# Kernel optimization log

Measured on AMD Instinct MI355X. Metric: run time of the kernel, lower is better.

## Reference

```python
import jax, jax.numpy as jnp
import numpy as np

B, S_IN, T_OUT, H, L, V = 64, 512, 64, 1024, 2, 1024


def setup_inputs() -> dict:
    key = jax.random.key(0)
    ks = iter(jax.random.split(key, 64))
    def p(shape, scale=0.02):
        return (jax.random.normal(next(ks), shape, jnp.float32) * scale)
    d = {"x": jax.random.normal(next(ks), (B, 2, S_IN), jnp.float32)}
    d["emb"] = p((V, H))
    for l in range(L):
        i = 2 if l == 0 else H
        d[f"enc_Wih{l}"] = p((3 * H, i)); d[f"enc_Whh{l}"] = p((3 * H, H))
        d[f"enc_bih{l}"] = p((3 * H,));   d[f"enc_bhh{l}"] = p((3 * H,))
        d[f"dec_Wih{l}"] = p((H, H));     d[f"dec_Whh{l}"] = p((H, H))
        d[f"dec_bih{l}"] = p((H,));       d[f"dec_bhh{l}"] = p((H,))
    d["hq_W"] = p((H, H)); d["hq_b"] = p((H,))
    d["comb_W"] = p((H, 2 * H)); d["comb_b"] = p((H,))
    d["fc_W"] = p((V, H)); d["fc_b"] = p((V,))
    return d


def _gru_layer(x_seq, Wih, Whh, bih, bhh):
    # x_seq: [B,T,I] -> (outputs [B,T,H], h_T [B,H]). PyTorch GRU gate order r,z,n.
    xp = jnp.einsum('bti,gi->btg', x_seq, Wih) + bih  # [B,T,3H]
    h0 = jnp.zeros((x_seq.shape[0], Whh.shape[1]), x_seq.dtype)
    def step(h, xpt):
        hp = h @ Whh.T + bhh
        xr, xz, xn = jnp.split(xpt, 3, axis=-1)
        hr, hz, hn = jnp.split(hp, 3, axis=-1)
        r = jax.nn.sigmoid(xr + hr)
        z = jax.nn.sigmoid(xz + hz)
        n = jnp.tanh(xn + r * hn)
        h = (1.0 - z) * n + z * h
        return h, h
    hT, ys = jax.lax.scan(step, h0, jnp.swapaxes(xp, 0, 1))
    return jnp.swapaxes(ys, 0, 1), hT


def _forward(x, emb,
             enc_Wih0, enc_Whh0, enc_bih0, enc_bhh0,
             enc_Wih1, enc_Whh1, enc_bih1, enc_bhh1,
             dec_Wih0, dec_Whh0, dec_bih0, dec_bhh0,
             dec_Wih1, dec_Whh1, dec_bih1, dec_bhh1,
             hq_W, hq_b, comb_W, comb_b, fc_W, fc_b):
    enc_params = [(enc_Wih0, enc_Whh0, enc_bih0, enc_bhh0),
                  (enc_Wih1, enc_Whh1, enc_bih1, enc_bhh1)]
    dec_params = [(dec_Wih0, dec_Whh0, dec_bih0, dec_bhh0),
                  (dec_Wih1, dec_Whh1, dec_bih1, dec_bhh1)]
    # ---- encoder: GRU over x permuted to [B, S_in, 2] ----
    seq = jnp.transpose(x, (0, 2, 1)).astype(jnp.float32)
    h_enc = []
    for (Wih, Whh, bih, bhh) in enc_params:
        seq, hT = _gru_layer(seq, Wih, Whh, bih, bhh)
        h_enc.append(hT)
    enc_outs = seq                      # [B, S_in, H]
    hidden0 = jnp.stack(h_enc, axis=0)  # [L, B, H]

    tok0 = jnp.zeros((B,), jnp.int32)
    def dec_step(carry, _):
        tok, hid = carry
        inp = emb[tok]                  # [B, H]
        new_h = []
        for l, (Wih, Whh, bih, bhh) in enumerate(dec_params):
            h = jnp.tanh(inp @ Wih.T + bih + hid[l] @ Whh.T + bhh)
            new_h.append(h)
            inp = h
        hid = jnp.stack(new_h, axis=0)
        q = inp @ hq_W.T + hq_b                          # [B, H]
        scores = jnp.einsum('bsh,bh->bs', enc_outs, q)   # [B, S_in]
        aw = jax.nn.softmax(scores, axis=1)
        att = jnp.einsum('bs,bsh->bh', aw, enc_outs)     # [B, H]
        logits = jnp.concatenate([inp, att], axis=-1) @ comb_W.T + comb_b
        logits = logits @ fc_W.T + fc_b                  # [B, V]
        tok = jnp.argmax(logits, axis=-1).astype(jnp.int32)
        return (tok, hid), (logits, aw)
    (_, hidden), (logits_t, aw_t) = jax.lax.scan(dec_step, (tok0, hidden0), None, length=T_OUT)
    vec_out = jnp.swapaxes(logits_t, 0, 1)   # [B, T_out, V]
    attn = aw_t[-1][:, None, :]              # [B, 1, S_in] (last step, as in source)
    return vec_out, hidden, attn


def reference(x, emb,
              enc_Wih0, enc_Whh0, enc_bih0, enc_bhh0,
              enc_Wih1, enc_Whh1, enc_bih1, enc_bhh1,
              dec_Wih0, dec_Whh0, dec_bih0, dec_bhh0,
              dec_Wih1, dec_Whh1, dec_bih1, dec_bhh1,
              hq_W, hq_b, comb_W, comb_b, fc_W, fc_b):
    return _forward(x, emb,
                    enc_Wih0, enc_Whh0, enc_bih0, enc_bhh0,
                    enc_Wih1, enc_Whh1, enc_bih1, enc_bhh1,
                    dec_Wih0, dec_Whh0, dec_bih0, dec_bhh0,
                    dec_Wih1, dec_Whh1, dec_bih1, dec_bhh1,
                    hq_W, hq_b, comb_W, comb_b, fc_W, fc_b)
```

## Files before the change

### kernel.cpp

```cpp
#include <hip/hip_runtime.h>
#include <stdint.h>


#define BB 64
#define SS 512
#define TT 64
#define HH 1024
#define VV 1024
#define BH 65536
#define SH 524288
#define OFF_HID  4194304
#define OFF_ATTN 4325376

typedef _Float16 half8  __attribute__((ext_vector_type(8)));
typedef float    floatx4 __attribute__((ext_vector_type(4)));

struct P {
  const float *x, *emb;
  const float *eWih0, *eWhh0, *ebih0, *ebhh0;
  const float *dWih0, *dWhh0, *dbih0, *dbhh0;
  const float *eWih1, *eWhh1, *ebih1, *ebhh1;
  const float *dWih1, *dWhh1, *dbih1, *dbhh1;
  const float *hqW, *hqb, *combW, *combb, *fcW, *fcb;
  uint32_t* enc_i;
  _Float16 *W0h,*W0l;
  _Float16 *W1h,*W1l;
  _Float16 *embh,*embl,*T0h,*T0l;
  _Float16 *wih0dh,*wih0dl,*wih1dh,*wih1dl,*whh0dh,*whh0dl,*whh1dh,*whh1dl;
  _Float16 *hqh,*hql,*combh,*combl,*fch,*fcl;
  _Float16 *h0h,*h0l,*h1h,*h1l;
  _Float16 *dh0h,*dh0l,*dh1h,*dh1l;
  _Float16 *cath,*catl;
  _Float16 *ch,*cl;
  float *u0,*u1,*w1x,*q;
  float *attp_o;
  float *attp_ml;
  float *sc63;
  unsigned long long* amax;
  float* dout;
};

struct GSet { const _Float16 *Wh, *Wl, *Ah, *Al; const float *bias; float *out; };

__device__ __forceinline__ void splitf(float x, _Float16& hi, _Float16& lo){
  _Float16 h = (_Float16)x; hi = h;
  lo = (_Float16)((x - (float)h) * 2048.0f);
}
__device__ __forceinline__ float reconf(_Float16 hi, _Float16 lo){
  return fmaf((float)lo, 1.0f/2048.0f, (float)hi);
}
__device__ __forceinline__ float recon_u32(uint32_t w){
  float hi = (float)__builtin_bit_cast(_Float16, (unsigned short)(w & 0xffffu));
  float lo = (float)__builtin_bit_cast(_Float16, (unsigned short)(w >> 16));
  return fmaf(lo, 1.0f/2048.0f, hi);
}
__device__ __forceinline__ uint32_t pack_pair(float x){
  _Float16 hi, lo; splitf(x, hi, lo);
  return (uint32_t)__builtin_bit_cast(unsigned short, hi)
       | ((uint32_t)__builtin_bit_cast(unsigned short, lo) << 16);
}
__device__ __forceinline__ unsigned ordf(float f){
  unsigned u = __float_as_uint(f);
  return (u & 0x80000000u) ? ~u : (u | 0x80000000u);
}

template<int NT, int KH, bool SPLIT>
__device__ __forceinline__ void gemm_core(
    const _Float16* __restrict__ Ah0, const _Float16* __restrict__ Al0,
    const _Float16* __restrict__ Ah1, const _Float16* __restrict__ Al1,
    int sA,
    const _Float16* __restrict__ Wh, const _Float16* __restrict__ Wl,
    int nrows, _Float16* ldsW, float* accOut)
{
  const int tid = threadIdx.x, lane = tid & 63, wave = tid >> 6;
  const int mA = (wave<<4) + (lane & 15);
  const int kb = ((lane>>4) << 3);
  const int wstride = KH << 10;
  floatx4 aH[NT], aM1[NT], aM2[NT];
  int ne[NT];
  const _Float16* bh_base[NT];
  const _Float16* bl_base[NT];
  #pragma unroll
  for (int nt=0; nt<NT; ++nt){
    int nn = (lane & 15) + (nt<<4);
    ne[nt] = nn < nrows ? nn : nrows - 1;
    bh_base[nt] = ldsW + ne[nt]*1032 + kb;
    aH[nt]  = floatx4{0.f,0.f,0.f,0.f};
    aM1[nt] = floatx4{0.f,0.f,0.f,0.f};
    aM2[nt] = floatx4{0.f,0.f,0.f,0.f};
  }
  #pragma unroll
  for (int kh=0; kh<KH; ++kh){
    __syncthreads();
    const int iters = (nrows*128 + 255) >> 8;
    for (int it=0; it<iters; ++it){
      int idx = tid + (it<<8);
      int row = idx >> 7, col = (idx & 127) << 3;
      if (row < nrows)
        *(half8*)(ldsW + row*1032 + col) =
            *(const half8*)(Wh + row*wstride + (kh<<10) + col);
    }
    __syncthreads();
    const _Float16* ah_p = ((KH==2 && kh==1) ? Ah1 : Ah0) + mA*sA + kb;
    const _Float16* al_p = ((KH==2 && kh==1) ? Al1 : Al0) + mA*sA + kb;
    #pragma unroll
    for (int nt=0; nt<NT; ++nt) bl_base[nt] = Wl + ne[nt]*wstride + (kh<<10) + kb;
    #pragma unroll 4
    for (int ks=0; ks<32; ++ks){
      half8 ah = *(const half8*)(ah_p + (ks<<5));
      half8 al = *(const half8*)(al_p + (ks<<5));
      #pragma unroll
      for (int nt=0; nt<NT; ++nt){
        half8 bh = *(const half8*)(bh_base[nt] + (ks<<5));
        half8 bl = *(const half8*)(bl_base[nt] + (ks<<5));
        aH[nt]  = __builtin_amdgcn_mfma_f32_16x16x32_f16(ah, bh, aH[nt],  0,0,0);
        aM1[nt] = __builtin_amdgcn_mfma_f32_16x16x32_f16(ah, bl, aM1[nt], 0,0,0);
        aM2[nt] = __builtin_amdgcn_mfma_f32_16x16x32_f16(al, bh, aM2[nt], 0,0,0);
      }
    }
    if (SPLIT){
      #pragma unroll
      for (int nt=0; nt<NT; ++nt){
        #pragma unroll
        for (int r=0;r<4;++r)
          accOut[(kh*NT + nt)*4 + r] = aH[nt][r] + (aM1[nt][r] + aM2[nt][r]) * (1.f/2048.f);
        aH[nt]  = floatx4{0.f,0.f,0.f,0.f};
        aM1[nt] = floatx4{0.f,0.f,0.f,0.f};
        aM2[nt] = floatx4{0.f,0.f,0.f,0.f};
      }
    }
  }
  if (!SPLIT){
    #pragma unroll
    for (int nt=0; nt<NT; ++nt)
      #pragma unroll
      for (int r=0;r<4;++r)
        accOut[nt*4 + r] = aH[nt][r] + (aM1[nt][r] + aM2[nt][r]) * (1.f/2048.f);
  }
}

__global__ __launch_bounds__(256) void k_split(const float* __restrict__ src,
                                               _Float16* dh, _Float16* dl, int n){
  for (int i = blockIdx.x*256 + threadIdx.x; i < n; i += gridDim.x*256){
    _Float16 hi,lo; splitf(src[i],hi,lo); dh[i]=hi; dl[i]=lo;
  }
}

__global__ __launch_bounds__(256) void k_rw0(P p){
  const int n = 128*24*1024;
  for (int i = blockIdx.x*256 + threadIdx.x; i < n; i += gridDim.x*256){
    int k = i & 1023; int rest = i >> 10; int rr = rest % 24; int blk = rest / 24;
    int grow = (rr>>3)*1024 + (blk<<3) + (rr&7);
    _Float16 hi,lo; splitf(p.eWhh0[grow*1024 + k],hi,lo);
    p.W0h[i]=hi; p.W0l[i]=lo;
  }
}
__global__ __launch_bounds__(256) void k_rw1(P p){
  const int n = 128*24*2048;
  for (int i = blockIdx.x*256 + threadIdx.x; i < n; i += gridDim.x*256){
    int k = i & 2047; int rest = i >> 11; int rr = rest % 24; int blk = rest / 24;
    int grow = (rr>>3)*1024 + (blk<<3) + (rr&7);
    float v = (k < 1024) ? p.eWhh1[grow*1024 + k] : p.eWih1[grow*1024 + (k-1024)];
    _Float16 hi,lo; splitf(v,hi,lo);
    p.W1h[i]=hi; p.W1l[i]=lo;
  }
}
__global__ __launch_bounds__(256) void k_zero(P p){
  int i = blockIdx.x*256 + threadIdx.x;
  p.h1h[i] = (_Float16)0.f; p.h1l[i] = (_Float16)0.f;
  p.h0h[BH + i] = (_Float16)0.f; p.h0l[BH + i] = (_Float16)0.f;
}
__global__ __launch_bounds__(256) void k_t0(P p){
  __shared__ _Float16 ldsW[16*1032];
  const int ns = blockIdx.x & 63, mc = blockIdx.x >> 6;
  float acc[4];
  gemm_core<1,1,false>(p.embh + mc*65536, p.embl + mc*65536, nullptr, nullptr, 1024,
                       p.wih0dh + ns*16*1024, p.wih0dl + ns*16*1024, 16, ldsW, acc);
  const int lane = threadIdx.x & 63, wave = threadIdx.x >> 6;
  const int n = lane & 15, col = (ns<<4) + n;
  const float bv = p.dbih0[col];
  #pragma unroll
  for (int r=0;r<4;++r){
    int v = mc*64 + (wave<<4) + ((lane>>4)<<2) + r;
    _Float16 hi,lo; splitf(acc[r] + bv, hi, lo);
    p.T0h[v*1024 + col] = hi; p.T0l[v*1024 + col] = lo;
  }
}

__global__ __launch_bounds__(256) void k_enc(P p, int e){
  const int tid = threadIdx.x, lane = tid & 63, wave = tid >> 6;
  const bool is0 = blockIdx.x < 128;
  if (is0 && e >= 512) return;
  if (!is0 && e < 1) return;
  const int blk = is0 ? blockIdx.x : blockIdx.x - 128;
  const int j0 = blk << 3;

  __shared__ _Float16 ldsW[24*1032];
  __shared__ float ldsG[2][24][68];
  __shared__ float ldsC[24][4];

  if (tid < 24){
    int grow = (tid>>3)*1024 + j0 + (tid & 7);
    if (is0){
      ldsC[tid][0] = p.eWih0[grow*2+0];
      ldsC[tid][1] = p.eWih0[grow*2+1];
      ldsC[tid][2] = p.ebih0[grow];
      ldsC[tid][3] = p.ebhh0[grow];
    } else {
      ldsC[tid][0] = p.ebih1[grow];
      ldsC[tid][1] = p.ebhh1[grow];
    }
  }

  const int cur = e & 1, prv = cur ^ 1;
  float acc[16];
  if (is0){
    gemm_core<2,1,true>(p.h0h + prv*BH, p.h0l + prv*BH, nullptr, nullptr, 1024,
                        p.W0h + blk*24*1024, p.W0l + blk*24*1024, 24, ldsW, acc);
    #pragma unroll
    for (int nt=0; nt<2; ++nt){
      int n = (lane & 15) + (nt<<4);
      if (n < 24){
        #pragma unroll
        for (int r=0;r<4;++r)
          ldsG[0][n][(wave<<4)+((lane>>4)<<2)+r] = acc[nt*4+r];
      }
    }
  } else {
    gemm_core<2,2,true>(p.h1h + prv*BH, p.h1l + prv*BH,
                        p.h0h + prv*BH, p.h0l + prv*BH, 1024,
                        p.W1h + blk*24*2048, p.W1l + blk*24*2048, 24, ldsW, acc);
    #pragma unroll
    for (int kh=0; kh<2; ++kh){
      #pragma unroll
      for (int nt=0; nt<2; ++nt){
        int n = (lane & 15) + (nt<<4);
        if (n < 24){
          #pragma unroll
          for (int r=0;r<4;++r)
            ldsG[kh][n][(wave<<4)+((lane>>4)<<2)+r] = acc[(kh*2+nt)*4+r];
        }
      }
    }
  }
  __syncthreads();

  #pragma unroll
  for (int it=0; it<2; ++it){
    int idx = tid + (it<<8);
    int b = idx & 63, j = idx >> 6;
    int col = j0 + j;
    if (is0){
      int t = e;
      float hr = ldsG[0][j][b]    + ldsC[j][3];
      float hz = ldsG[0][8+j][b]  + ldsC[8+j][3];
      float hn = ldsG[0][16+j][b] + ldsC[16+j][3];
      float x0 = p.x[b*1024 + t], x1 = p.x[b*1024 + 512 + t];
      float xr = fmaf(x0, ldsC[j][0],    fmaf(x1, ldsC[j][1],    ldsC[j][2]));
      float xz = fmaf(x0, ldsC[8+j][0],  fmaf(x1, ldsC[8+j][1],  ldsC[8+j][2]));
      float xn = fmaf(x0, ldsC[16+j][0], fmaf(x1, ldsC[16+j][1], ldsC[16+j][2]));
      float rg = 1.0f/(1.0f + expf(-(xr+hr)));
      float zg = 1.0f/(1.0f + expf(-(xz+hz)));
      float ng = tanhf(xn + rg*hn);
      float hold = reconf(p.h0h[prv*BH + b*1024 + col], p.h0l[prv*BH + b*1024 + col]);
      float hnew = (1.0f - zg)*ng + zg*hold;
      _Float16 hi,lo; splitf(hnew,hi,lo);
      p.h0h[cur*BH + b*1024 + col] = hi;
      p.h0l[cur*BH + b*1024 + col] = lo;
    } else {
      int t = e - 1;
      float hr = ldsG[0][j][b]    + ldsC[j][1];
      float hz = ldsG[0][8+j][b]  + ldsC[8+j][1];
      float hn = ldsG[0][16+j][b] + ldsC[16+j][1];
      float xr = ldsG[1][j][b]    + ldsC[j][0];
      float xz = ldsG[1][8+j][b]  + ldsC[8+j][0];
      float xn = ldsG[1][16+j][b] + ldsC[16+j][0];
      float rg = 1.0f/(1.0f + expf(-(xr+hr)));
      float zg = 1.0f/(1.0f + expf(-(xz+hz)));
      float ng = tanhf(xn + rg*hn);
      float hold = reconf(p.h1h[prv*BH + b*1024 + col], p.h1l[prv*BH + b*1024 + col]);
      float hnew = (1.0f - zg)*ng + zg*hold;
      _Float16 hi,lo; splitf(hnew,hi,lo);
      p.h1h[cur*BH + b*1024 + col] = hi;
      p.h1l[cur*BH + b*1024 + col] = lo;
      p.enc_i[b*SH + t*1024 + col] = pack_pair(hnew);
    }
  }
}

__global__ __launch_bounds__(256) void k_dgemm2(GSet a, GSet b){
  const int tid = threadIdx.x, lane = tid & 63, wave = tid >> 6;
  const GSet g = blockIdx.x < 128 ? a : b;
  const int blk = blockIdx.x & 127;
  __shared__ _Float16 ldsW[8*1032];
  float acc[4];
  gemm_core<1,1,false>(g.Ah, g.Al, nullptr, nullptr, 1024,
                       g.Wh + blk*8*1024, g.Wl + blk*8*1024, 8, ldsW, acc);
  int n = lane & 15;
  if (n < 8){
    int col = (blk<<3) + n;
    float bv = g.bias[col];
    #pragma unroll
    for (int r=0;r<4;++r){
      int m = (wave<<4)+((lane>>4)<<2)+r;
      g.out[m*1024 + col] = acc[r] + bv;
    }
  }
}

__global__ __launch_bounds__(256) void k_dec0(P p, int t){
  const int tid = threadIdx.x, b = blockIdx.x;
  __shared__ unsigned long long red[256];
  unsigned long long v = 0;
  if (t > 0 && tid < 128) v = p.amax[b*128 + tid];
  red[tid] = v; __syncthreads();
  for (int off=128; off>=1; off>>=1){
    if (tid < off){ unsigned long long o = red[tid+off]; if (o > red[tid]) red[tid] = o; }
    __syncthreads();
  }
  const int tokb = (t > 0) ? (1023 - (int)(red[0] & 0xffffffffULL)) : 0;
  #pragma unroll
  for (int i=0;i<4;++i){
    int h = tid + (i<<8);
    float val = tanhf(reconf(p.T0h[tokb*1024+h], p.T0l[tokb*1024+h]) + p.u0[b*1024+h]);
    _Float16 hi,lo; splitf(val,hi,lo);
    p.dh0h[b*1024+h]=hi; p.dh0l[b*1024+h]=lo;
  }
}
__global__ __launch_bounds__(256) void k_dec2(P p){
  const int tid = threadIdx.x, b = blockIdx.x;
  #pragma unroll
  for (int i=0;i<4;++i){
    int h = tid + (i<<8);
    float val = tanhf(p.w1x[b*1024+h] + p.u1[b*1024+h]);
    _Float16 hi,lo; splitf(val,hi,lo);
    p.dh1h[b*1024+h]=hi; p.dh1l[b*1024+h]=lo;
    p.cath[b*2048+h]=hi; p.catl[b*2048+h]=lo;
  }
}
__global__ __launch_bounds__(256) void k_flash(P p, int t){
  const int tid = threadIdx.x, lane = tid & 63, wave = tid >> 6;
  const int b = blockIdx.x >> 1, half = blockIdx.x & 1;
  const int s0 = half << 8;
  const bool last = (t == 63);
  float qv[16];
  #pragma unroll
  for (int i=0;i<16;++i) qv[i] = p.q[b*1024 + (i<<6) + lane];
  float ov[16];
  #pragma unroll
  for (int i=0;i<16;++i) ov[i] = 0.f;
  float mrun = -3.0e38f, lrun = 0.f;
  for (int si=0; si<64; ++si){
    int s = s0 + (wave<<6) + si;
    const uint32_t* ep = p.enc_i + b*SH + s*1024 + lane;
    float ef[16]; float partial = 0.f;
    #pragma unroll
    for (int i=0;i<16;++i){
      ef[i] = recon_u32(ep[i<<6]);
      partial = fmaf(ef[i], qv[i], partial);
    }
    #pragma unroll
    for (int off=32; off; off>>=1) partial += __shfl_xor(partial, off, 64);
    if (last && lane == 0) p.sc63[b*512 + s] = partial;
    float mnew = fmaxf(mrun, partial);
    float fac = __expf(mrun - mnew);
    float w   = __expf(partial - mnew);
    lrun = fmaf(lrun, fac, w);
    #pragma unroll
    for (int i=0;i<16;++i) ov[i] = fmaf(ov[i], fac, w*ef[i]);
    mrun = mnew;
  }
  __shared__ float ldsO[4][1024];
  __shared__ float ldsM[4], ldsL2[4];
  #pragma unroll
  for (int i=0;i<16;++i) ldsO[wave][(i<<6)+lane] = ov[i];
  if (lane == 0){ ldsM[wave] = mrun; ldsL2[wave] = lrun; }
  __syncthreads();
  float M = fmaxf(fmaxf(ldsM[0],ldsM[1]), fmaxf(ldsM[2],ldsM[3]));
  float f0 = __expf(ldsM[0]-M), f1 = __expf(ldsM[1]-M),
        f2 = __expf(ldsM[2]-M), f3 = __expf(ldsM[3]-M);
  if (tid == 0){
    p.attp_ml[b*4 + half*2 + 0] = M;
    p.attp_ml[b*4 + half*2 + 1] = f0*ldsL2[0] + f1*ldsL2[1] + f2*ldsL2[2] + f3*ldsL2[3];
  }
  #pragma unroll
  for (int i=0;i<4;++i){
    int h = tid + (i<<8);
    p.attp_o[(b*2+half)*1024 + h] =
        f0*ldsO[0][h] + f1*ldsO[1][h] + f2*ldsO[2][h] + f3*ldsO[3][h];
  }
}
__global__ __launch_bounds__(256) void k_dec5(P p, int t){
  const int tid = threadIdx.x, b = blockIdx.x;
  float m0 = p.attp_ml[b*4+0], l0 = p.attp_ml[b*4+1];
  float m1 = p.attp_ml[b*4+2], l1 = p.attp_ml[b*4+3];
  float M = fmaxf(m0,m1);
  float f0 = expf(m0-M), f1 = expf(m1-M);
  float invL = 1.0f/(f0*l0 + f1*l1);
  #pragma unroll
  for (int i=0;i<4;++i){
    int h = tid + (i<<8);
    float o = (f0*p.attp_o[(b*2+0)*1024+h] + f1*p.attp_o[(b*2+1)*1024+h]) * invL;
    _Float16 hi,lo; splitf(o,hi,lo);
    p.cath[b*2048 + 1024 + h] = hi; p.catl[b*2048 + 1024 + h] = lo;
  }
  if (t == 63){
    #pragma unroll
    for (int i=0;i<2;++i){
      int s = tid + (i<<8);
      p.dout[OFF_ATTN + b*512 + s] = expf(p.sc63[b*512+s] - M) * invL;
    }
  }
}
__global__ __launch_bounds__(256) void k_comb(P p){
  const int tid = threadIdx.x, lane = tid & 63, wave = tid >> 6;
  const int blk = blockIdx.x;
  __shared__ _Float16 ldsW[8*1032];
  float acc[4];
  gemm_core<1,2,false>(p.cath, p.catl, p.cath + 1024, p.catl + 1024, 2048,
                       p.combh + blk*8*2048, p.combl + blk*8*2048, 8, ldsW, acc);
  int n = lane & 15;
  if (n < 8){
    int col = (blk<<3) + n;
    float bv = p.combb[col];
    #pragma unroll
    for (int r=0;r<4;++r){
      int m = (wave<<4)+((lane>>4)<<2)+r;
      _Float16 hi,lo; splitf(acc[r] + bv, hi, lo);
      p.ch[m*1024 + col] = hi; p.cl[m*1024 + col] = lo;
    }
  }
}
__global__ __launch_bounds__(256) void k_fc(P p, int t){
  const int tid = threadIdx.x, lane = tid & 63, wave = tid >> 6;
  const int blk = blockIdx.x;
  __shared__ _Float16 ldsW[8*1032];
  __shared__ float ldsL[8][68];
  float acc[4];
  gemm_core<1,1,false>(p.ch, p.cl, nullptr, nullptr, 1024,
                       p.fch + blk*8*1024, p.fcl + blk*8*1024, 8, ldsW, acc);
  int n = lane & 15;
  if (n < 8){
    int col = (blk<<3) + n;
    float bv = p.fcb[col];
    #pragma unroll
    for (int r=0;r<4;++r){
      int m = (wave<<4)+((lane>>4)<<2)+r;
      float val = acc[r] + bv;
      p.dout[m*65536 + t*1024 + col] = val;
      ldsL[n][m] = val;
    }
  }
  __syncthreads();
  if (tid < 64){
    int b = tid; float best = -3.0e38f; int bi = 0;
    #pragma unroll
    for (int jj=0; jj<8; ++jj){
      float v = ldsL[jj][b];
      if (v > best){ best = v; bi = jj; }
    }
    unsigned long long pk = ((unsigned long long)ordf(best) << 32)
                          | (unsigned)(1023 - ((blk<<3) + bi));
    p.amax[b*128 + blk] = pk;
  }
}
__global__ __launch_bounds__(256) void k_hidden(P p){
  int idx = blockIdx.x*256 + threadIdx.x;
  int i = idx & 65535;
  float v = (idx >> 16) ? reconf(p.dh1h[i], p.dh1l[i]) : reconf(p.dh0h[i], p.dh0l[i]);
  p.dout[OFF_HID + idx] = v;
}

extern "C" void kernel_launch(void* const* d_in, const int* in_sizes, int n_in,
                              void* d_out, int out_size, void* d_ws, size_t ws_size,
                              hipStream_t stream)
{
  (void)in_sizes; (void)n_in; (void)out_size;
  P p;
  p.x     = (const float*)d_in[0];  p.emb   = (const float*)d_in[1];
  p.eWih0 = (const float*)d_in[2];  p.eWhh0 = (const float*)d_in[3];
  p.ebih0 = (const float*)d_in[4];  p.ebhh0 = (const float*)d_in[5];
  p.dWih0 = (const float*)d_in[6];  p.dWhh0 = (const float*)d_in[7];
  p.dbih0 = (const float*)d_in[8];  p.dbhh0 = (const float*)d_in[9];
  p.eWih1 = (const float*)d_in[10]; p.eWhh1 = (const float*)d_in[11];
  p.ebih1 = (const float*)d_in[12]; p.ebhh1 = (const float*)d_in[13];
  p.dWih1 = (const float*)d_in[14]; p.dWhh1 = (const float*)d_in[15];
  p.dbih1 = (const float*)d_in[16]; p.dbhh1 = (const float*)d_in[17];
  p.hqW   = (const float*)d_in[18]; p.hqb   = (const float*)d_in[19];
  p.combW = (const float*)d_in[20]; p.combb = (const float*)d_in[21];
  p.fcW   = (const float*)d_in[22]; p.fcb   = (const float*)d_in[23];
  p.dout  = (float*)d_out;

  char* base = (char*)d_ws; size_t off = 0;
  auto alloc = [&](size_t bytes)->char*{
    char* r = base + off; off = (off + bytes + 255) & ~(size_t)255; return r;
  };
  p.enc_i = (uint32_t*)alloc(33554432ULL*4);
  p.W0h = (_Float16*)alloc(3145728ULL*2);  p.W0l = (_Float16*)alloc(3145728ULL*2);
  p.W1h = (_Float16*)alloc(6291456ULL*2);  p.W1l = (_Float16*)alloc(6291456ULL*2);
  p.embh = (_Float16*)alloc(1048576ULL*2); p.embl = (_Float16*)alloc(1048576ULL*2);
  p.T0h  = (_Float16*)alloc(1048576ULL*2); p.T0l  = (_Float16*)alloc(1048576ULL*2);
  p.wih0dh=(_Float16*)alloc(1048576ULL*2); p.wih0dl=(_Float16*)alloc(1048576ULL*2);
  p.wih1dh=(_Float16*)alloc(1048576ULL*2); p.wih1dl=(_Float16*)alloc(1048576ULL*2);
  p.whh0dh=(_Float16*)alloc(1048576ULL*2); p.whh0dl=(_Float16*)alloc(1048576ULL*2);
  p.whh1dh=(_Float16*)alloc(1048576ULL*2); p.whh1dl=(_Float16*)alloc(1048576ULL*2);
  p.hqh  = (_Float16*)alloc(1048576ULL*2); p.hql  = (_Float16*)alloc(1048576ULL*2);
  p.combh= (_Float16*)alloc(2097152ULL*2); p.combl= (_Float16*)alloc(2097152ULL*2);
  p.fch  = (_Float16*)alloc(1048576ULL*2); p.fcl  = (_Float16*)alloc(1048576ULL*2);
  p.h0h  = (_Float16*)alloc(131072ULL*2);  p.h0l  = (_Float16*)alloc(131072ULL*2);
  p.h1h  = (_Float16*)alloc(131072ULL*2);  p.h1l  = (_Float16*)alloc(131072ULL*2);
  p.dh0h = (_Float16*)alloc(65536ULL*2);   p.dh0l = (_Float16*)alloc(65536ULL*2);
  p.dh1h = (_Float16*)alloc(65536ULL*2);   p.dh1l = (_Float16*)alloc(65536ULL*2);
  p.cath = (_Float16*)alloc(131072ULL*2);  p.catl = (_Float16*)alloc(131072ULL*2);
  p.ch   = (_Float16*)alloc(65536ULL*2);   p.cl   = (_Float16*)alloc(65536ULL*2);
  p.u0   = (float*)alloc(65536ULL*4);      p.u1   = (float*)alloc(65536ULL*4);
  p.w1x  = (float*)alloc(65536ULL*4);      p.q    = (float*)alloc(65536ULL*4);
  p.attp_o  = (float*)alloc(131072ULL*4);
  p.attp_ml = (float*)alloc(256ULL*4);
  p.sc63    = (float*)alloc(32768ULL*4);
  p.amax    = (unsigned long long*)alloc(8192ULL*8);
  if (off > ws_size) return;

  k_split<<<2048,256,0,stream>>>(p.emb,   p.embh,   p.embl,   1048576);
  k_split<<<2048,256,0,stream>>>(p.dWih0, p.wih0dh, p.wih0dl, 1048576);
  k_split<<<2048,256,0,stream>>>(p.dWih1, p.wih1dh, p.wih1dl, 1048576);
  k_split<<<2048,256,0,stream>>>(p.dWhh0, p.whh0dh, p.whh0dl, 1048576);
  k_split<<<2048,256,0,stream>>>(p.dWhh1, p.whh1dh, p.whh1dl, 1048576);
  k_split<<<2048,256,0,stream>>>(p.hqW,   p.hqh,    p.hql,    1048576);
  k_split<<<2048,256,0,stream>>>(p.combW, p.combh,  p.combl,  2097152);
  k_split<<<2048,256,0,stream>>>(p.fcW,   p.fch,    p.fcl,    1048576);
  k_rw0<<<4096,256,0,stream>>>(p);
  k_rw1<<<4096,256,0,stream>>>(p);
  k_zero<<<256,256,0,stream>>>(p);
  k_t0<<<1024,256,0,stream>>>(p);

  for (int e=0; e<=512; ++e) k_enc<<<256,256,0,stream>>>(p, e);

  {
    GSet a{p.whh0dh, p.whh0dl, p.h0h + BH, p.h0l + BH, p.dbhh0, p.u0};
    GSet b{p.whh1dh, p.whh1dl, p.h1h,      p.h1l,      p.dbhh1, p.u1};
    k_dgemm2<<<256,256,0,stream>>>(a, b);
  }
  GSet sK1a{p.wih1dh, p.wih1dl, p.dh0h, p.dh0l, p.dbih1, p.w1x};
  GSet sK1b{p.whh0dh, p.whh0dl, p.dh0h, p.dh0l, p.dbhh0, p.u0};
  GSet sK3a{p.hqh,    p.hql,    p.dh1h, p.dh1l, p.hqb,   p.q};
  GSet sK3b{p.whh1dh, p.whh1dl, p.dh1h, p.dh1l, p.dbhh1, p.u1};

  for (int t=0; t<64; ++t){
    k_dec0<<<64,256,0,stream>>>(p, t);
    k_dgemm2<<<256,256,0,stream>>>(sK1a, sK1b);
    k_dec2<<<64,256,0,stream>>>(p);
    k_dgemm2<<<256,256,0,stream>>>(sK3a, sK3b);
    k_flash<<<128,256,0,stream>>>(p, t);
    k_dec5<<<64,256,0,stream>>>(p, t);
    k_comb<<<128,256,0,stream>>>(p);
    k_fc<<<128,256,0,stream>>>(p, t);
  }
  k_hidden<<<512,256,0,stream>>>(p);
}
```

Before: 30.33 ms.

## Halve per-block encoder tile to 4 hidden units, doubling grid to 512 blocks

The encoder step kernel now gives each block 4 hidden columns (12 gate rows) instead of 8 (24), and launches 512 blocks instead of 256. The weights are re-laid out to match. The generic gemm_core is replaced by an inline MFMA loop over a single 16-wide N tile, of which only 12 columns are used. For layer 1, only the high halves of the weights are staged in LDS and the low halves are read straight from global memory, so LDS stays within budget with launch_bounds(256,2). The goal is more parallelism per sequential step, at the cost of wasted MFMA columns and extra global reads.

```diff
diff --git a/kernel.cpp b/kernel.cpp
--- a/kernel.cpp
+++ b/kernel.cpp
@@ -147,19 +147,19 @@
 }
 
 __global__ __launch_bounds__(256) void k_rw0(P p){
-  const int n = 128*24*1024;
+  const int n = 256*12*1024;
   for (int i = blockIdx.x*256 + threadIdx.x; i < n; i += gridDim.x*256){
-    int k = i & 1023; int rest = i >> 10; int rr = rest % 24; int blk = rest / 24;
-    int grow = (rr>>3)*1024 + (blk<<3) + (rr&7);
+    int k = i & 1023; int rest = i >> 10; int rr = rest % 12; int blk = rest / 12;
+    int grow = (rr>>2)*1024 + (blk<<2) + (rr&3);
     _Float16 hi,lo; splitf(p.eWhh0[grow*1024 + k],hi,lo);
     p.W0h[i]=hi; p.W0l[i]=lo;
   }
 }
 __global__ __launch_bounds__(256) void k_rw1(P p){
-  const int n = 128*24*2048;
+  const int n = 256*12*2048;
   for (int i = blockIdx.x*256 + threadIdx.x; i < n; i += gridDim.x*256){
-    int k = i & 2047; int rest = i >> 11; int rr = rest % 24; int blk = rest / 24;
-    int grow = (rr>>3)*1024 + (blk<<3) + (rr&7);
+    int k = i & 2047; int rest = i >> 11; int rr = rest % 12; int blk = rest / 12;
+    int grow = (rr>>2)*1024 + (blk<<2) + (rr&3);
     float v = (k < 1024) ? p.eWhh1[grow*1024 + k] : p.eWih1[grow*1024 + (k-1024)];
     _Float16 hi,lo; splitf(v,hi,lo);
     p.W1h[i]=hi; p.W1l[i]=lo;
@@ -187,78 +187,87 @@
   }
 }
 
-__global__ __launch_bounds__(256) void k_enc(P p, int e){
+__global__ __launch_bounds__(256,2) void k_enc(P p, int e){
+  __shared__ _Float16 ldsW[24768];
+  __shared__ float ldsG[2*12*68];
+  __shared__ float ldsC[12*4];
   const int tid = threadIdx.x, lane = tid & 63, wave = tid >> 6;
-  const bool is0 = blockIdx.x < 128;
+  const bool is0 = blockIdx.x < 256;
   if (is0 && e >= 512) return;
   if (!is0 && e < 1) return;
-  const int blk = is0 ? blockIdx.x : blockIdx.x - 128;
-  const int j0 = blk << 3;
-
-  __shared__ _Float16 ldsW[24*1032];
-  __shared__ float ldsG[2][24][68];
-  __shared__ float ldsC[24][4];
-
-  if (tid < 24){
-    int grow = (tid>>3)*1024 + j0 + (tid & 7);
+  const int blk = is0 ? (int)blockIdx.x : (int)blockIdx.x - 256;
+  const int j0 = blk << 2;
+
+  if (is0){
+    const _Float16* gh = p.W0h + blk*12*1024;
+    const _Float16* gl = p.W0l + blk*12*1024;
+    _Float16* Wl = ldsW + 12*1032;
+    for (int it = tid; it < 12*128; it += 256){
+      int row = it >> 7, col = (it & 127) << 3;
+      *(half8*)(ldsW + row*1032 + col) = *(const half8*)(gh + row*1024 + col);
+      *(half8*)(Wl   + row*1032 + col) = *(const half8*)(gl + row*1024 + col);
+    }
+  } else {
+    const _Float16* gh = p.W1h + blk*12*2048;
+    for (int it = tid; it < 12*256; it += 256){
+      int row = it >> 8, col = (it & 255) << 3;
+      *(half8*)(ldsW + row*2056 + col) = *(const half8*)(gh + row*2048 + col);
+    }
+  }
+  if (tid < 12){
+    int grow = (tid>>2)*1024 + j0 + (tid & 3);
     if (is0){
-      ldsC[tid][0] = p.eWih0[grow*2+0];
-      ldsC[tid][1] = p.eWih0[grow*2+1];
-      ldsC[tid][2] = p.ebih0[grow];
-      ldsC[tid][3] = p.ebhh0[grow];
+      ldsC[tid*4+0] = p.eWih0[grow*2+0];
+      ldsC[tid*4+1] = p.eWih0[grow*2+1];
+      ldsC[tid*4+2] = p.ebih0[grow];
+      ldsC[tid*4+3] = p.ebhh0[grow];
     } else {
-      ldsC[tid][0] = p.ebih1[grow];
-      ldsC[tid][1] = p.ebhh1[grow];
-    }
-  }
+      ldsC[tid*4+0] = p.ebih1[grow];
+      ldsC[tid*4+1] = p.ebhh1[grow];
+    }
+  }
+  __syncthreads();
 
   const int cur = e & 1, prv = cur ^ 1;
-  float acc[16];
+  const int mA = (wave<<4) + (lane & 15);
+  const int kb = ((lane>>4) << 3);
+  const int nn = lane & 15;
+  const int ne = nn < 12 ? nn : 11;
+  const int b_ep = tid & 63, c_ep = tid >> 6;
+  const int col_ep = j0 + c_ep;
+
   if (is0){
-    gemm_core<2,1,true>(p.h0h + prv*BH, p.h0l + prv*BH, nullptr, nullptr, 1024,
-                        p.W0h + blk*24*1024, p.W0l + blk*24*1024, 24, ldsW, acc);
-    #pragma unroll
-    for (int nt=0; nt<2; ++nt){
-      int n = (lane & 15) + (nt<<4);
-      if (n < 24){
-        #pragma unroll
-        for (int r=0;r<4;++r)
-          ldsG[0][n][(wave<<4)+((lane>>4)<<2)+r] = acc[nt*4+r];
-      }
-    }
-  } else {
-    gemm_core<2,2,true>(p.h1h + prv*BH, p.h1l + prv*BH,
-                        p.h0h + prv*BH, p.h0l + prv*BH, 1024,
-                        p.W1h + blk*24*2048, p.W1l + blk*24*2048, 24, ldsW, acc);
-    #pragma unroll
-    for (int kh=0; kh<2; ++kh){
+    floatx4 aH{0.f,0.f,0.f,0.f}, aM1{0.f,0.f,0.f,0.f}, aM2{0.f,0.f,0.f,0.f};
+    const _Float16* ah_p = p.h0h + prv*BH + mA*1024 + kb;
+    const _Float16* al_p = p.h0l + prv*BH + mA*1024 + kb;
+    const _Float16* bh_p = ldsW + ne*1032 + kb;
+    const _Float16* bl_p = ldsW + 12*1032 + ne*1032 + kb;
+    #pragma unroll 4
+    for (int ks=0; ks<32; ++ks){
+      half8 ah = *(const half8*)(ah_p + (ks<<5));
+      half8 al = *(const half8*)(al_p + (ks<<5));
+      half8 bh = *(const half8*)(bh_p + (ks<<5));
+      half8 bl = *(const half8*)(bl_p + (ks<<5));
+      aH  = __builtin_amdgcn_mfma_f32_16x16x32_f16(ah, bh, aH,  0,0,0);
+      aM1 = __builtin_amdgcn_mfma_f32_16x16x32_f16(ah, bl, aM1, 0,0,0);
+      aM2 = __builtin_amdgcn_mfma_f32_16x16x32_f16(al, bh, aM2, 0,0,0);
+    }
+    if (nn < 12){
       #pragma unroll
-      for (int nt=0; nt<2; ++nt){
-        int n = (lane & 15) + (nt<<4);
-        if (n < 24){
-          #pragma unroll
-          for (int r=0;r<4;++r)
-            ldsG[kh][n][(wave<<4)+((lane>>4)<<2)+r] = acc[(kh*2+nt)*4+r];
-        }
-      }
-    }
-  }
-  __syncthreads();
-
-  #pragma unroll
-  for (int it=0; it<2; ++it){
-    int idx = tid + (it<<8);
-    int b = idx & 63, j = idx >> 6;
-    int col = j0 + j;
-    if (is0){
-      int t = e;
-      float hr = ldsG[0][j][b]    + ldsC[j][3];
-      float hz = ldsG[0][8+j][b]  + ldsC[8+j][3];
-      float hn = ldsG[0][16+j][b] + ldsC[16+j][3];
-      float x0 = p.x[b*1024 + t], x1 = p.x[b*1024 + 512 + t];
-      float xr = fmaf(x0, ldsC[j][0],    fmaf(x1, ldsC[j][1],    ldsC[j][2]));
-      float xz = fmaf(x0, ldsC[8+j][0],  fmaf(x1, ldsC[8+j][1],  ldsC[8+j][2]));
-      float xn = fmaf(x0, ldsC[16+j][0], fmaf(x1, ldsC[16+j][1], ldsC[16+j][2]));
+      for (int r=0;r<4;++r)
+        ldsG[nn*68 + (wave<<4)+((lane>>4)<<2)+r] =
+            aH[r] + (aM1[r] + aM2[r]) * (1.f/2048.f);
+    }
+    __syncthreads();
+    {
+      const int b = b_ep, c = c_ep, col = col_ep;
+      float hr = ldsG[c*68+b]     + ldsC[c*4+3];
+      float hz = ldsG[(4+c)*68+b] + ldsC[(4+c)*4+3];
+      float hn = ldsG[(8+c)*68+b] + ldsC[(8+c)*4+3];
+      float x0 = p.x[b*1024 + e], x1 = p.x[b*1024 + 512 + e];
+      float xr = fmaf(x0, ldsC[c*4+0],     fmaf(x1, ldsC[c*4+1],     ldsC[c*4+2]));
+      float xz = fmaf(x0, ldsC[(4+c)*4+0], fmaf(x1, ldsC[(4+c)*4+1], ldsC[(4+c)*4+2]));
+      float xn = fmaf(x0, ldsC[(8+c)*4+0], fmaf(x1, ldsC[(8+c)*4+1], ldsC[(8+c)*4+2]));
       float rg = 1.0f/(1.0f + expf(-(xr+hr)));
       float zg = 1.0f/(1.0f + expf(-(xz+hz)));
       float ng = tanhf(xn + rg*hn);
@@ -267,14 +276,42 @@
       _Float16 hi,lo; splitf(hnew,hi,lo);
       p.h0h[cur*BH + b*1024 + col] = hi;
       p.h0l[cur*BH + b*1024 + col] = lo;
-    } else {
-      int t = e - 1;
-      float hr = ldsG[0][j][b]    + ldsC[j][1];
-      float hz = ldsG[0][8+j][b]  + ldsC[8+j][1];
-      float hn = ldsG[0][16+j][b] + ldsC[16+j][1];
-      float xr = ldsG[1][j][b]    + ldsC[j][0];
-      float xz = ldsG[1][8+j][b]  + ldsC[8+j][0];
-      float xn = ldsG[1][16+j][b] + ldsC[16+j][0];
+    }
+  } else {
+    #pragma unroll
+    for (int kh=0; kh<2; ++kh){
+      floatx4 aH{0.f,0.f,0.f,0.f}, aM1{0.f,0.f,0.f,0.f}, aM2{0.f,0.f,0.f,0.f};
+      const _Float16* ah_p = (kh ? p.h0h : p.h1h) + prv*BH + mA*1024 + kb;
+      const _Float16* al_p = (kh ? p.h0l : p.h1l) + prv*BH + mA*1024 + kb;
+      const _Float16* bh_p = ldsW + ne*2056 + (kh<<10) + kb;
+      const _Float16* bl_p = p.W1l + blk*12*2048 + ne*2048 + (kh<<10) + kb;
+      #pragma unroll 4
+      for (int ks=0; ks<32; ++ks){
+        half8 ah = *(const half8*)(ah_p + (ks<<5));
+        half8 al = *(const half8*)(al_p + (ks<<5));
+        half8 bh = *(const half8*)(bh_p + (ks<<5));
+        half8 bl = *(const half8*)(bl_p + (ks<<5));
+        aH  = __builtin_amdgcn_mfma_f32_16x16x32_f16(ah, bh, aH,  0,0,0);
+        aM1 = __builtin_amdgcn_mfma_f32_16x16x32_f16(ah, bl, aM1, 0,0,0);
+        aM2 = __builtin_amdgcn_mfma_f32_16x16x32_f16(al, bh, aM2, 0,0,0);
+      }
+      if (nn < 12){
+        #pragma unroll
+        for (int r=0;r<4;++r)
+          ldsG[(kh*12+nn)*68 + (wave<<4)+((lane>>4)<<2)+r] =
+              aH[r] + (aM1[r] + aM2[r]) * (1.f/2048.f);
+      }
+    }
+    __syncthreads();
+    {
+      const int b = b_ep, c = c_ep, col = col_ep;
+      const int t = e - 1;
+      float hr = ldsG[c*68+b]        + ldsC[c*4+1];
+      float hz = ldsG[(4+c)*68+b]    + ldsC[(4+c)*4+1];
+      float hn = ldsG[(8+c)*68+b]    + ldsC[(8+c)*4+1];
+      float xr = ldsG[(12+c)*68+b]   + ldsC[c*4+0];
+      float xz = ldsG[(12+4+c)*68+b] + ldsC[(4+c)*4+0];
+      float xn = ldsG[(12+8+c)*68+b] + ldsC[(8+c)*4+0];
       float rg = 1.0f/(1.0f + expf(-(xr+hr)));
       float zg = 1.0f/(1.0f + expf(-(xz+hz)));
       float ng = tanhf(xn + rg*hn);
@@ -534,7 +571,7 @@
   k_zero<<<256,256,0,stream>>>(p);
   k_t0<<<1024,256,0,stream>>>(p);
 
-  for (int e=0; e<=512; ++e) k_enc<<<256,256,0,stream>>>(p, e);
+  for (int e=0; e<=512; ++e) k_enc<<<512,256,0,stream>>>(p, e);
 
   {
     GSet a{p.whh0dh, p.whh0dl, p.h0h + BH, p.h0l + BH, p.dbhh0, p.u0};
```

New measurement: 28.65 ms. 5.5% less time.
